# Performance work log

Measured on AMD Instinct MI355X. Metric: run time of the kernel, lower is better.

## Reference

```python
import jax, jax.numpy as jnp
import numpy as np

N_POINTS = 1440   # number of detector angles (thetas)
N_INT = 4000      # trapezoid integration samples along each ray
N_GRID = 4096     # SoS field is (N_GRID, N_GRID)
GRID_LO, GRID_HI = -0.06, 0.06
R_BODY = 0.05
V0 = 1500.0


def setup_inputs() -> dict:
    key = jax.random.key(0)
    k1, k2, k3 = jax.random.split(key, 3)
    # query point strictly inside the body circle (r < R_body)
    x = jnp.float32(0.012)
    y = jnp.float32(-0.007)
    # speed-of-sound field ~ water SoS with heterogeneity, strictly positive
    SoS = (1480.0 + 40.0 * jax.random.uniform(k3, (N_GRID, N_GRID))).astype(jnp.float32)
    thetas = jnp.linspace(0.0, 2.0 * jnp.pi, N_POINTS, dtype=jnp.float32).reshape(-1, 1)
    steps = jnp.linspace(0.0, 1.0, N_INT, dtype=jnp.float32).reshape(1, -1)
    x_vec = jnp.linspace(GRID_LO, GRID_HI, N_GRID, dtype=jnp.float32)
    dx = x_vec[1] - x_vec[0]
    return {
        "x": x, "y": y, "SoS": SoS,
        "thetas": thetas, "steps": steps,
        "x0": x_vec[0], "y0": x_vec[0], "dx": dx, "dy": dx,
        "R_body": jnp.float32(R_BODY), "v0": jnp.float32(V0),
    }


def reference(x, y, SoS, thetas, steps, x0, y0, dx, dy, R_body, v0):
    # polar coords of query point; note torch code uses atan2(x, y)
    r = jnp.sqrt(x * x + y * y)
    phi = jnp.arctan2(x, y)
    s = r * jnp.sin(thetas - phi)                      # (P,1)
    arg = jnp.maximum(R_body * R_body - s * s, 0.0)    # shared, >0 when r<R_body
    sqrt_arg = jnp.sqrt(arg)
    l_in = sqrt_arg + r * jnp.cos(thetas - phi)
    l_out = 2.0 * sqrt_arg * (jnp.cos(phi - thetas) >= 0.0).astype(sqrt_arg.dtype)
    l = jnp.where(r < R_body, l_in, l_out)             # (P,1) chord lengths

    xs = l * steps                                     # (P,N) arc-length samples
    px = x - xs * jnp.sin(thetas)                      # (P,N) sample positions
    py = y - xs * jnp.cos(thetas)
    x_index = jnp.round((px - x0) / dx).astype(jnp.int32)
    y_index = jnp.round((py - y0) / dy).astype(jnp.int32)
    # gather: negative row index (-y_index) wraps from the end, as in torch/numpy
    vals = 1.0 - v0 / SoS[-y_index, x_index]           # (P,N)
    # trapezoid over non-uniformly labeled x = l*steps (uniform per row)
    dseg = jnp.diff(xs, axis=1)                        # (P,N-1)
    wf = jnp.sum(0.5 * (vals[:, :-1] + vals[:, 1:]) * dseg, axis=1)
    return thetas.reshape(-1), wf
```

## Files before the change

### kernel.cpp

```cpp
#include <hip/hip_runtime.h>

#define N_POINTS 1440
#define N_INT    4000
#define N_GRID   4096
#define BLOCK    256
#define MAIN_ITERS (N_INT / BLOCK)
#define REMAIN     (N_INT - MAIN_ITERS * BLOCK)

__global__ __launch_bounds__(256) void wavefront_sos_kernel(
    const float* __restrict__ xp,
    const float* __restrict__ yp,
    const float* __restrict__ SoS,
    const float* __restrict__ thetas,
    const float* __restrict__ steps,
    const float* __restrict__ x0p,
    const float* __restrict__ y0p,
    const float* __restrict__ dxp,
    const float* __restrict__ dyp,
    const float* __restrict__ Rp,
    const float* __restrict__ v0p,
    float* __restrict__ out)
{
    const int b = blockIdx.x;
    const int p = (b & 7) * (N_POINTS / 8) + (b >> 3);

    const float x  = xp[0];
    const float y  = yp[0];
    const float x0 = x0p[0];
    const float y0 = y0p[0];
    const float dx = dxp[0];
    const float dy = dyp[0];
    const float Rb = Rp[0];
    const float v0 = v0p[0];

    const float theta = thetas[p];

    const float r   = sqrtf(x * x + y * y);
    const float phi = atan2f(x, y);
    const float st  = sinf(theta);
    const float ct  = cosf(theta);

    const float s     = r * sinf(theta - phi);
    const float arg   = fmaxf(Rb * Rb - s * s, 0.0f);
    const float sq    = sqrtf(arg);
    const float l_in  = sq + r * cosf(theta - phi);
    const float l_out = 2.0f * sq * (cosf(phi - theta) >= 0.0f ? 1.0f : 0.0f);
    const float l     = (r < Rb) ? l_in : l_out;

    const float ds = 1.0f / 3999.0f;
    const float Ax = (x - x0) / dx;
    const float Bx = l * st / dx;
    const float Ay = (y - y0) / dy;
    const float By = l * ct / dy;

    const float s_base = (float)threadIdx.x * ds;
    const float fx0 = fmaf(-Bx, s_base, Ax);
    const float fy0 = fmaf(-By, s_base, Ay);
    const float nBxd = -Bx * (256.0f * ds);
    const float nByd = -By * (256.0f * ds);

    __shared__ float endv[2];
    __shared__ float wave_sums[4];

    float acc = 0.0f;

#define SAMPLE(itf, vdst)                                            \
    {                                                                \
        const float fx = fmaf((itf), nBxd, fx0);                     \
        const float fy = fmaf((itf), nByd, fy0);                     \
        const int xi = (int)rintf(fx);                               \
        const int yi = (int)rintf(fy);                               \
        const int idx = ((N_GRID - yi) << 12) + xi;                  \
        const float sosv = SoS[idx];                                 \
        vdst = fmaf(-v0, __builtin_amdgcn_rcpf(sosv), 1.0f);         \
    }

#pragma unroll
    for (int it = 0; it < MAIN_ITERS; ++it) {
        float v;
        SAMPLE((float)it, v);
        if (it == 0 && threadIdx.x == 0) endv[0] = v;
        acc += v;
    }
    if (threadIdx.x < REMAIN) {
        float v;
        SAMPLE((float)MAIN_ITERS, v);
        if (threadIdx.x == REMAIN - 1) endv[1] = v;
        acc += v;
    }
#undef SAMPLE

    for (int off = 32; off > 0; off >>= 1)
        acc += __shfl_down(acc, off, 64);

    const int lane = threadIdx.x & 63;
    const int wave = threadIdx.x >> 6;
    if (lane == 0) wave_sums[wave] = acc;
    __syncthreads();

    if (threadIdx.x == 0) {
        const float total = wave_sums[0] + wave_sums[1] + wave_sums[2] + wave_sums[3];
        const float wf = l * ds * (total - 0.5f * (endv[0] + endv[1]));
        out[p] = theta;
        out[N_POINTS + p] = wf;
    }
}

extern "C" void kernel_launch(void* const* d_in, const int* in_sizes, int n_in,
                              void* d_out, int out_size, void* d_ws, size_t ws_size,
                              hipStream_t stream) {
    (void)in_sizes; (void)n_in; (void)out_size; (void)d_ws; (void)ws_size;

    const float* xp     = (const float*)d_in[0];
    const float* yp     = (const float*)d_in[1];
    const float* SoS    = (const float*)d_in[2];
    const float* thetas = (const float*)d_in[3];
    const float* steps  = (const float*)d_in[4];
    const float* x0p    = (const float*)d_in[5];
    const float* y0p    = (const float*)d_in[6];
    const float* dxp    = (const float*)d_in[7];
    const float* dyp    = (const float*)d_in[8];
    const float* Rp     = (const float*)d_in[9];
    const float* v0p    = (const float*)d_in[10];

    float* out = (float*)d_out;

    wavefront_sos_kernel<<<N_POINTS, BLOCK, 0, stream>>>(
        xp, yp, SoS, thetas, steps, x0p, y0p, dxp, dyp, Rp, v0p, out);
}
```

Measured before the change: 120.3 us.

## Split each ray across two blocks with a second kernel for endpoints and combine

Each ray's 4000 samples are now split into two halves handled by separate blocks (2880 blocks total), with partial sums written to workspace. A second small kernel recomputes ray geometry, gathers the two endpoint samples, and combines the partials into the trapezoid result. This raises parallelism and shortens the per-block dependent gather chain, but adds a second kernel launch, a workspace round trip, and duplicated geometry work. The accumulation is also fused into a single FMA per sample.

```diff
diff --git a/kernel.cpp b/kernel.cpp
--- a/kernel.cpp
+++ b/kernel.cpp
@@ -4,37 +4,15 @@
 #define N_INT    4000
 #define N_GRID   4096
 #define BLOCK    256
-#define MAIN_ITERS (N_INT / BLOCK)
-#define REMAIN     (N_INT - MAIN_ITERS * BLOCK)
+#define HALF     2000
+#define H_ITERS  (HALF / BLOCK)
+#define H_REMAIN (HALF - H_ITERS * BLOCK)
 
-__global__ __launch_bounds__(256) void wavefront_sos_kernel(
-    const float* __restrict__ xp,
-    const float* __restrict__ yp,
-    const float* __restrict__ SoS,
-    const float* __restrict__ thetas,
-    const float* __restrict__ steps,
-    const float* __restrict__ x0p,
-    const float* __restrict__ y0p,
-    const float* __restrict__ dxp,
-    const float* __restrict__ dyp,
-    const float* __restrict__ Rp,
-    const float* __restrict__ v0p,
-    float* __restrict__ out)
+__device__ __forceinline__ void ray_geometry(
+    float x, float y, float x0, float y0, float dx, float dy,
+    float Rb, float theta,
+    float& l, float& Ax, float& Bx, float& Ay, float& By)
 {
-    const int b = blockIdx.x;
-    const int p = (b & 7) * (N_POINTS / 8) + (b >> 3);
-
-    const float x  = xp[0];
-    const float y  = yp[0];
-    const float x0 = x0p[0];
-    const float y0 = y0p[0];
-    const float dx = dxp[0];
-    const float dy = dyp[0];
-    const float Rb = Rp[0];
-    const float v0 = v0p[0];
-
-    const float theta = thetas[p];
-
     const float r   = sqrtf(x * x + y * y);
     const float phi = atan2f(x, y);
     const float st  = sinf(theta);
@@ -45,26 +23,53 @@
     const float sq    = sqrtf(arg);
     const float l_in  = sq + r * cosf(theta - phi);
     const float l_out = 2.0f * sq * (cosf(phi - theta) >= 0.0f ? 1.0f : 0.0f);
-    const float l     = (r < Rb) ? l_in : l_out;
+    l = (r < Rb) ? l_in : l_out;
+
+    Ax = (x - x0) / dx;
+    Bx = l * st / dx;
+    Ay = (y - y0) / dy;
+    By = l * ct / dy;
+}
+
+__global__ __launch_bounds__(256) void wavefront_partial_kernel(
+    const float* __restrict__ xp,
+    const float* __restrict__ yp,
+    const float* __restrict__ SoS,
+    const float* __restrict__ thetas,
+    const float* __restrict__ x0p,
+    const float* __restrict__ y0p,
+    const float* __restrict__ dxp,
+    const float* __restrict__ dyp,
+    const float* __restrict__ Rp,
+    const float* __restrict__ v0p,
+    float* __restrict__ ws_acc)
+{
+    const int b = blockIdx.x;
+    const int h = (b < N_POINTS) ? 0 : 1;
+    const int i = (b < N_POINTS) ? b : b - N_POINTS;
+    const int p = (i & 7) * (N_POINTS / 8) + (i >> 3);
+
+    const float x  = xp[0];
+    const float y  = yp[0];
+    const float Rb = Rp[0];
+    const float v0 = v0p[0];
+
+    const float theta = thetas[p];
+
+    float l, Ax, Bx, Ay, By;
+    ray_geometry(x, y, x0p[0], y0p[0], dxp[0], dyp[0], Rb, theta,
+                 l, Ax, Bx, Ay, By);
 
     const float ds = 1.0f / 3999.0f;
-    const float Ax = (x - x0) / dx;
-    const float Bx = l * st / dx;
-    const float Ay = (y - y0) / dy;
-    const float By = l * ct / dy;
-
-    const float s_base = (float)threadIdx.x * ds;
+    const float s_base = (float)(h * HALF + (int)threadIdx.x) * ds;
     const float fx0 = fmaf(-Bx, s_base, Ax);
     const float fy0 = fmaf(-By, s_base, Ay);
     const float nBxd = -Bx * (256.0f * ds);
     const float nByd = -By * (256.0f * ds);
 
-    __shared__ float endv[2];
-    __shared__ float wave_sums[4];
-
     float acc = 0.0f;
 
-#define SAMPLE(itf, vdst)                                            \
+#define SAMPLE(itf)                                                  \
     {                                                                \
         const float fx = fmaf((itf), nBxd, fx0);                     \
         const float fy = fmaf((itf), nByd, fy0);                     \
@@ -72,50 +77,87 @@
         const int yi = (int)rintf(fy);                               \
         const int idx = ((N_GRID - yi) << 12) + xi;                  \
         const float sosv = SoS[idx];                                 \
-        vdst = fmaf(-v0, __builtin_amdgcn_rcpf(sosv), 1.0f);         \
+        acc = fmaf(-v0, __builtin_amdgcn_rcpf(sosv), acc + 1.0f);    \
     }
 
 #pragma unroll
-    for (int it = 0; it < MAIN_ITERS; ++it) {
-        float v;
-        SAMPLE((float)it, v);
-        if (it == 0 && threadIdx.x == 0) endv[0] = v;
-        acc += v;
+    for (int it = 0; it < H_ITERS; ++it) {
+        SAMPLE((float)it);
     }
-    if (threadIdx.x < REMAIN) {
-        float v;
-        SAMPLE((float)MAIN_ITERS, v);
-        if (threadIdx.x == REMAIN - 1) endv[1] = v;
-        acc += v;
+    if (threadIdx.x < H_REMAIN) {
+        SAMPLE((float)H_ITERS);
     }
 #undef SAMPLE
 
     for (int off = 32; off > 0; off >>= 1)
         acc += __shfl_down(acc, off, 64);
 
+    __shared__ float wave_sums[4];
     const int lane = threadIdx.x & 63;
     const int wave = threadIdx.x >> 6;
     if (lane == 0) wave_sums[wave] = acc;
     __syncthreads();
 
-    if (threadIdx.x == 0) {
-        const float total = wave_sums[0] + wave_sums[1] + wave_sums[2] + wave_sums[3];
-        const float wf = l * ds * (total - 0.5f * (endv[0] + endv[1]));
-        out[p] = theta;
-        out[N_POINTS + p] = wf;
-    }
+    if (threadIdx.x == 0)
+        ws_acc[h * N_POINTS + p] =
+            wave_sums[0] + wave_sums[1] + wave_sums[2] + wave_sums[3];
+}
+
+__global__ __launch_bounds__(256) void wavefront_final_kernel(
+    const float* __restrict__ xp,
+    const float* __restrict__ yp,
+    const float* __restrict__ SoS,
+    const float* __restrict__ thetas,
+    const float* __restrict__ x0p,
+    const float* __restrict__ y0p,
+    const float* __restrict__ dxp,
+    const float* __restrict__ dyp,
+    const float* __restrict__ Rp,
+    const float* __restrict__ v0p,
+    const float* __restrict__ ws_acc,
+    float* __restrict__ out)
+{
+    const int p = blockIdx.x * blockDim.x + threadIdx.x;
+    if (p >= N_POINTS) return;
+
+    const float x  = xp[0];
+    const float y  = yp[0];
+    const float Rb = Rp[0];
+    const float v0 = v0p[0];
+
+    const float theta = thetas[p];
+
+    float l, Ax, Bx, Ay, By;
+    ray_geometry(x, y, x0p[0], y0p[0], dxp[0], dyp[0], Rb, theta,
+                 l, Ax, Bx, Ay, By);
+
+    const int xi0 = (int)rintf(Ax);
+    const int yi0 = (int)rintf(Ay);
+    const float sos0 = SoS[((N_GRID - yi0) << 12) + xi0];
+    const float v_first = fmaf(-v0, __builtin_amdgcn_rcpf(sos0), 1.0f);
+
+    const int xiN = (int)rintf(fmaf(-Bx, 1.0f, Ax));
+    const int yiN = (int)rintf(fmaf(-By, 1.0f, Ay));
+    const float sosN = SoS[((N_GRID - yiN) << 12) + xiN];
+    const float v_last = fmaf(-v0, __builtin_amdgcn_rcpf(sosN), 1.0f);
+
+    const float ds = 1.0f / 3999.0f;
+    const float total = ws_acc[p] + ws_acc[N_POINTS + p];
+    const float wf = l * ds * (total - 0.5f * (v_first + v_last));
+
+    out[p] = theta;
+    out[N_POINTS + p] = wf;
 }
 
 extern "C" void kernel_launch(void* const* d_in, const int* in_sizes, int n_in,
                               void* d_out, int out_size, void* d_ws, size_t ws_size,
                               hipStream_t stream) {
-    (void)in_sizes; (void)n_in; (void)out_size; (void)d_ws; (void)ws_size;
+    (void)in_sizes; (void)n_in; (void)out_size; (void)ws_size;
 
     const float* xp     = (const float*)d_in[0];
     const float* yp     = (const float*)d_in[1];
     const float* SoS    = (const float*)d_in[2];
     const float* thetas = (const float*)d_in[3];
-    const float* steps  = (const float*)d_in[4];
     const float* x0p    = (const float*)d_in[5];
     const float* y0p    = (const float*)d_in[6];
     const float* dxp    = (const float*)d_in[7];
@@ -123,8 +165,12 @@
     const float* Rp     = (const float*)d_in[9];
     const float* v0p    = (const float*)d_in[10];
 
-    float* out = (float*)d_out;
+    float* ws_acc = (float*)d_ws;
+    float* out    = (float*)d_out;
 
-    wavefront_sos_kernel<<<N_POINTS, BLOCK, 0, stream>>>(
-        xp, yp, SoS, thetas, steps, x0p, y0p, dxp, dyp, Rp, v0p, out);
+    wavefront_partial_kernel<<<2 * N_POINTS, BLOCK, 0, stream>>>(
+        xp, yp, SoS, thetas, x0p, y0p, dxp, dyp, Rp, v0p, ws_acc);
+
+    wavefront_final_kernel<<<(N_POINTS + BLOCK - 1) / BLOCK, BLOCK, 0, stream>>>(
+        xp, yp, SoS, thetas, x0p, y0p, dxp, dyp, Rp, v0p, ws_acc, out);
 }
```

Measured after the change: 121.9 us. About the same (+1.4%).
